# Performance work log

Hardware: AMD Instinct MI355X
Metric: run time of the kernel (lower is better)

## Reference

```python
import jax, jax.numpy as jnp
import numpy as np

B, T, D, H, C = 128, 1000, 40, 128, 8  # batch, time, input feats, hidden, classes


def _lstm_layer(x, Wih, Whh, bih, bhh):
    """Unidirectional LSTM over time. x: [B,T,Din] -> [B,T,H]. PyTorch gate order i,f,g,o."""
    Bn = x.shape[0]
    Hn = Whh.shape[1]
    b = bih + bhh
    def step(carry, xt):
        h, c = carry
        g = xt @ Wih.T + h @ Whh.T + b  # [B,4H]
        i, f, gg, o = jnp.split(g, 4, axis=-1)
        c = jax.nn.sigmoid(f) * c + jax.nn.sigmoid(i) * jnp.tanh(gg)
        h = jax.nn.sigmoid(o) * jnp.tanh(c)
        return (h, c), h
    h0 = jnp.zeros((Bn, Hn), x.dtype)
    _, hs = jax.lax.scan(step, (h0, h0), jnp.swapaxes(x, 0, 1))  # scan over time
    return jnp.swapaxes(hs, 0, 1)


def _bilstm_layer(x, pf, pb):
    fwd = _lstm_layer(x, *pf)
    bwd = jnp.flip(_lstm_layer(jnp.flip(x, 1), *pb), 1)
    return jnp.concatenate([fwd, bwd], axis=-1)  # [B,T,2H]


def setup_inputs() -> dict:
    key = jax.random.key(0)
    ks = jax.random.split(key, 16)
    s = 0.05
    def rn(k, shape):
        return jax.random.normal(k, shape, jnp.float32) * s
    inp = {"x": jax.random.normal(ks[0], (B, T, D), jnp.float32)}
    inp["ln_g"] = jnp.ones((D,), jnp.float32)
    inp["ln_b"] = jnp.zeros((D,), jnp.float32)
    dims = [D, 2 * H]  # layer-0 input feats, layer-1 input feats
    i = 1
    for l in range(2):
        for d in ("f", "b"):
            inp[f"Wih_{d}{l}"] = rn(ks[i], (4 * H, dims[l])); i += 1
            inp[f"Whh_{d}{l}"] = rn(ks[i], (4 * H, H)); i += 1
            inp[f"bih_{d}{l}"] = jnp.zeros((4 * H,), jnp.float32)
            inp[f"bhh_{d}{l}"] = jnp.zeros((4 * H,), jnp.float32)
    inp["attn_W1"] = rn(ks[i], (H, 2 * H)); i += 1
    inp["attn_b1"] = jnp.zeros((H,), jnp.float32)
    inp["attn_w2"] = rn(ks[i], (1, H)); i += 1
    inp["fc_W1"] = rn(ks[i], (H, 2 * H)); i += 1
    inp["fc_b1"] = jnp.zeros((H,), jnp.float32)
    inp["fc_W2"] = rn(ks[i], (C, H)); i += 1
    inp["fc_b2"] = jnp.zeros((C,), jnp.float32)
    return inp


def reference(x, ln_g, ln_b,
              Wih_f0, Whh_f0, bih_f0, bhh_f0, Wih_b0, Whh_b0, bih_b0, bhh_b0,
              Wih_f1, Whh_f1, bih_f1, bhh_f1, Wih_b1, Whh_b1, bih_b1, bhh_b1,
              attn_W1, attn_b1, attn_w2, fc_W1, fc_b1, fc_W2, fc_b2):
    # LayerNorm over feature dim (eps=1e-5, PyTorch default)
    mu = jnp.mean(x, axis=-1, keepdims=True)
    var = jnp.var(x, axis=-1, keepdims=True)
    xn = (x - mu) * jax.lax.rsqrt(var + 1e-5) * ln_g + ln_b
    # 2-layer bidirectional LSTM
    h = _bilstm_layer(xn, (Wih_f0, Whh_f0, bih_f0, bhh_f0), (Wih_b0, Whh_b0, bih_b0, bhh_b0))
    h = _bilstm_layer(h, (Wih_f1, Whh_f1, bih_f1, bhh_f1), (Wih_b1, Whh_b1, bih_b1, bhh_b1))
    # attention pooling: Linear-Tanh-Linear(no bias) -> softmax over time
    scores = jnp.tanh(h @ attn_W1.T + attn_b1) @ attn_w2[0]  # [B,T]
    w = jax.nn.softmax(scores, axis=1)
    ctx = jnp.einsum('bt,btd->bd', w, h)  # [B,2H]
    # MLP classifier head
    hid = jax.nn.relu(ctx @ fc_W1.T + fc_b1)
    return hid @ fc_W2.T + fc_b2  # [B,C] logits
```

## Files before the change

kernel.cpp:

```cpp
#include <hip/hip_runtime.h>

#define T_ 1000

__device__ __forceinline__ float sigf(float x) { return 1.0f / (1.0f + __expf(-x)); }
__device__ __forceinline__ float tanh_fast(float x) { return 1.0f - 2.0f / (1.0f + __expf(2.0f * x)); }
__device__ __forceinline__ float dot4(float4 a, float4 b) {
  return a.x * b.x + a.y * b.y + a.z * b.z + a.w * b.w;
}
__device__ __forceinline__ unsigned short f2bf(float f) {
  unsigned u = __float_as_uint(f);
  u = (u + 0x7fffu + ((u >> 16) & 1u)) >> 16;
  return (unsigned short)u;
}
__device__ __forceinline__ float bf2f(unsigned short h) {
  return __uint_as_float(((unsigned)h) << 16);
}
__device__ __forceinline__ float4 bf4_to_f4(ushort4 u) {
  float4 r;
  r.x = bf2f(u.x); r.y = bf2f(u.y); r.z = bf2f(u.z); r.w = bf2f(u.w);
  return r;
}

__global__ void bail_kernel(float* out, int n) {
  for (int i = threadIdx.x; i < n; i += 256) out[i] = 0.0f;
}

__global__ __launch_bounds__(512, 2) void rec0_kernel(
    const float* __restrict__ x,
    const float* __restrict__ ln_g, const float* __restrict__ ln_b,
    const float* __restrict__ Wih_f, const float* __restrict__ Whh_f,
    const float* __restrict__ bih_f, const float* __restrict__ bhh_f,
    const float* __restrict__ Wih_b, const float* __restrict__ Whh_b,
    const float* __restrict__ bih_b, const float* __restrict__ bhh_b,
    float* __restrict__ h0) {
  const int tid = threadIdx.x;
  const int j = tid & 127;
  const int p = tid >> 7;
  const int brow = blockIdx.x & 127;
  const int dir = blockIdx.x >> 7;
  const float* __restrict__ Wih = dir ? Wih_b : Wih_f;
  const float* __restrict__ Whh = dir ? Whh_b : Whh_f;
  const float* __restrict__ bih = dir ? bih_b : bih_f;
  const float* __restrict__ bhh = dir ? bhh_b : bhh_f;

  float4 wh[4][8];
  float4 wi[4][3];
#pragma unroll
  for (int g = 0; g < 4; ++g) {
    const int row = g * 128 + j;
    const float4* wr = (const float4*)(Whh + row * 128 + p * 32);
#pragma unroll
    for (int f = 0; f < 8; ++f) wh[g][f] = wr[f];
    const float* xr_ = Wih + row * 40;
#pragma unroll
    for (int f = 0; f < 3; ++f) {
      const int k0 = p * 12 + f * 4;
      float4 tv;
      tv.x = (k0 + 0 < 40) ? xr_[k0 + 0] : 0.0f;
      tv.y = (k0 + 1 < 40) ? xr_[k0 + 1] : 0.0f;
      tv.z = (k0 + 2 < 40) ? xr_[k0 + 2] : 0.0f;
      tv.w = (k0 + 3 < 40) ? xr_[k0 + 3] : 0.0f;
      wi[g][f] = tv;
    }
  }
  const float bias = bih[p * 128 + j] + bhh[p * 128 + j];
  const float b0 = (p == 0) ? bias : 0.0f;
  const float b1 = (p == 1) ? bias : 0.0f;
  const float b2 = (p == 2) ? bias : 0.0f;
  const float b3 = (p == 3) ? bias : 0.0f;

  __shared__ float4 h4[32];
  __shared__ float4 x4[12];
  __shared__ float4 part4[384];
  __shared__ float hring[8][128];

  float gj = 0.0f, bj = 0.0f;
  if (p == 1 && j < 40) { gj = ln_g[j]; bj = ln_b[j]; }

  if (tid < 32) h4[tid] = make_float4(0.f, 0.f, 0.f, 0.f);
  if (tid >= 40 && tid < 48) ((float*)x4)[tid] = 0.0f;
  __syncthreads();

  const long xbase = (long)brow * T_ * 40;
  float xr[8];
  if (p == 1 && j < 64) {
    const long tA = dir ? (T_ - 1) : 0;
    float v = (j < 40) ? x[xbase + tA * 40 + j] : 0.0f;
    float s1 = v, s2 = v * v;
#pragma unroll
    for (int m = 32; m; m >>= 1) {
      s1 += __shfl_xor(s1, m, 64);
      s2 += __shfl_xor(s2, m, 64);
    }
    const float mu = s1 * (1.0f / 40.0f);
    const float var = s2 * (1.0f / 40.0f) - mu * mu;
    const float rs = rsqrtf(var + 1e-5f);
    if (j < 40) ((float*)x4)[j] = (v - mu) * rs * gj + bj;
#pragma unroll
    for (int v8 = 0; v8 < 8; ++v8) {
      const int tr = 1 + v8;
      xr[v8] = 0.0f;
      if (j < 40 && tr < T_) {
        const long tt = dir ? (T_ - 1 - tr) : tr;
        xr[v8] = x[xbase + tt * 40 + j];
      }
    }
  }
  float c = 0.0f;
  __syncthreads();

  const long hbase = (long)brow * T_ * 256;
  for (int sb = 0; sb < 125; ++sb) {
#pragma unroll
    for (int u = 0; u < 8; ++u) {
      const int t = sb * 8 + u;
      float a0 = b0, a1 = b1, a2 = b2, a3 = b3;
#pragma unroll
      for (int f = 0; f < 3; ++f) {
        const float4 xv = x4[p * 3 + f];
        a0 += dot4(xv, wi[0][f]);
        a1 += dot4(xv, wi[1][f]);
        a2 += dot4(xv, wi[2][f]);
        a3 += dot4(xv, wi[3][f]);
      }
#pragma unroll
      for (int f = 0; f < 8; ++f) {
        const float4 hv = h4[p * 8 + f];
        a0 += dot4(hv, wh[0][f]);
        a1 += dot4(hv, wh[1][f]);
        a2 += dot4(hv, wh[2][f]);
        a3 += dot4(hv, wh[3][f]);
      }
      if (p) part4[(p - 1) * 128 + j] = make_float4(a0, a1, a2, a3);
      __syncthreads();
      if (!p) {
        const float4 q0 = part4[j], q1 = part4[128 + j], q2 = part4[256 + j];
        a0 += q0.x + q1.x + q2.x;
        a1 += q0.y + q1.y + q2.y;
        a2 += q0.z + q1.z + q2.z;
        a3 += q0.w + q1.w + q2.w;
        const float ig = sigf(a0);
        const float fg = sigf(a1);
        const float gg = tanh_fast(a2);
        const float og = sigf(a3);
        c = fg * c + ig * gg;
        const float hv = og * tanh_fast(c);
        ((float*)h4)[j] = hv;
        hring[u][j] = hv;
      } else if (p == 1 && j < 64) {
        if (t + 1 < T_) {
          float v = xr[u];
          float s1 = v, s2 = v * v;
#pragma unroll
          for (int m = 32; m; m >>= 1) {
            s1 += __shfl_xor(s1, m, 64);
            s2 += __shfl_xor(s2, m, 64);
          }
          const float mu = s1 * (1.0f / 40.0f);
          const float var = s2 * (1.0f / 40.0f) - mu * mu;
          const float rs = rsqrtf(var + 1e-5f);
          if (j < 40) ((float*)x4)[j] = (v - mu) * rs * gj + bj;
        }
      }
      __syncthreads();
      if (u == 7) {
        if (p == 3) {
#pragma unroll
          for (int v = 0; v < 8; ++v) {
            const int ts = sb * 8 + v;
            const int te = dir ? (T_ - 1 - ts) : ts;
            h0[hbase + (long)te * 256 + dir * 128 + j] = hring[v][j];
          }
        } else if (p == 1 && j < 64) {
#pragma unroll
          for (int v = 0; v < 8; ++v) {
            const int tr = sb * 8 + 9 + v;
            xr[v] = 0.0f;
            if (j < 40 && tr < T_) {
              const long tt = dir ? (T_ - 1 - tr) : tr;
              xr[v] = x[xbase + tt * 40 + j];
            }
          }
        }
      }
    }
  }
}

__global__ __launch_bounds__(512, 2) void rec1_kernel(
    const float* __restrict__ xw_f, const float* __restrict__ xw_b,
    const float* __restrict__ Whh_f, const float* __restrict__ bih_f, const float* __restrict__ bhh_f,
    const float* __restrict__ Whh_b, const float* __restrict__ bih_b, const float* __restrict__ bhh_b,
    unsigned short* __restrict__ h1b, float* __restrict__ state,
    int Tc, int t0f, int t0b, int first) {
  const int tid = threadIdx.x;
  const int j = tid & 127;
  const int p = tid >> 7;
  const int brow = blockIdx.x & 127;
  const int dir = blockIdx.x >> 7;
  const float* __restrict__ xw = dir ? xw_b : xw_f;
  const float* __restrict__ Whh = dir ? Whh_b : Whh_f;
  const float* __restrict__ bih = dir ? bih_b : bih_f;
  const float* __restrict__ bhh = dir ? bhh_b : bhh_f;
  const int t0 = dir ? t0b : t0f;

  float4 wh[4][8];
#pragma unroll
  for (int g = 0; g < 4; ++g) {
    const float4* wr = (const float4*)(Whh + (g * 128 + j) * 128 + p * 32);
#pragma unroll
    for (int f = 0; f < 8; ++f) wh[g][f] = wr[f];
  }
  const int myrow = p * 128 + j;
  const float bias = bih[myrow] + bhh[myrow];

  __shared__ float4 h4[32];
  __shared__ float4 part4[384];
  __shared__ float hring[8][128];
  float* sblk = state + (long)blockIdx.x * 256;
  float c = 0.0f;
  if (first) {
    if (tid < 32) h4[tid] = make_float4(0.f, 0.f, 0.f, 0.f);
  } else {
    if (tid < 128) ((float*)h4)[tid] = sblk[tid];
    if (!p) c = sblk[128 + j];
  }
  const long gbase = (long)brow * Tc;
  float xr[8];
#pragma unroll
  for (int v = 0; v < 8; ++v) {
    const int sn = v;
    xr[v] = 0.0f;
    if (sn < Tc) {
      const int tr = dir ? (Tc - 1 - sn) : sn;
      xr[v] = xw[(gbase + tr) * 512 + myrow];
    }
  }
  __syncthreads();

  const int nSB = (Tc + 7) / 8;
  for (int sb = 0; sb < nSB; ++sb) {
#pragma unroll
    for (int u = 0; u < 8; ++u) {
      const int s = sb * 8 + u;
      if (s >= Tc) break;
      float a0 = 0.f, a1 = 0.f, a2 = 0.f, a3 = 0.f;
#pragma unroll
      for (int f = 0; f < 8; ++f) {
        const float4 hv = h4[p * 8 + f];
        a0 += dot4(hv, wh[0][f]);
        a1 += dot4(hv, wh[1][f]);
        a2 += dot4(hv, wh[2][f]);
        a3 += dot4(hv, wh[3][f]);
      }
      const float xin = xr[u] + bias;
      if (p == 0) a0 += xin;
      else if (p == 1) a1 += xin;
      else if (p == 2) a2 += xin;
      else a3 += xin;
      if (p) part4[(p - 1) * 128 + j] = make_float4(a0, a1, a2, a3);
      __syncthreads();
      if (!p) {
        const float4 q0 = part4[j], q1 = part4[128 + j], q2 = part4[256 + j];
        a0 += q0.x + q1.x + q2.x;
        a1 += q0.y + q1.y + q2.y;
        a2 += q0.z + q1.z + q2.z;
        a3 += q0.w + q1.w + q2.w;
        const float ig = sigf(a0);
        const float fg = sigf(a1);
        const float gg = tanh_fast(a2);
        const float og = sigf(a3);
        c = fg * c + ig * gg;
        const float hv = og * tanh_fast(c);
        ((float*)h4)[j] = hv;
        hring[u][j] = hv;
      }
      __syncthreads();
      if (u == 7 || s + 1 == Tc) {
        if (p == 3) {
#pragma unroll
          for (int v = 0; v < 8; ++v) {
            const int s2 = sb * 8 + v;
            if (s2 <= s) {
              const int tt = dir ? (Tc - 1 - s2) : s2;
              h1b[((long)brow * T_ + (t0 + tt)) * 256 + dir * 128 + j] = f2bf(hring[v][j]);
            }
          }
        }
#pragma unroll
        for (int v = 0; v < 8; ++v) {
          const int sn = s + 1 + v;
          xr[v] = 0.0f;
          if (sn < Tc) {
            const int tr = dir ? (Tc - 1 - sn) : sn;
            xr[v] = xw[(gbase + tr) * 512 + myrow];
          }
        }
      }
    }
  }
  if (tid < 128) sblk[tid] = ((float*)h4)[tid];
  if (!p) sblk[128 + j] = c;
}

__global__ __launch_bounds__(256, 2) void gemm_xw1(
    const float* __restrict__ h0,
    const float* __restrict__ Wf, const float* __restrict__ Wb,
    float* __restrict__ xwf, float* __restrict__ xwb,
    int Tc, int t0f, int t0b) {
  __shared__ float As[64 * 36];
  __shared__ float Bs[128 * 36];
  __shared__ int rowbase[64];
  const int tid = threadIdx.x;
  const int tx = tid & 15, ty = tid >> 4;
  const int r0 = blockIdx.x * 64;
  const int jt = blockIdx.y;
  const int dir = jt >> 2;
  const int nh = jt & 3;
  const float* __restrict__ W = dir ? Wb : Wf;
  float* __restrict__ out = dir ? xwb : xwf;
  const int jbase = nh * 128;
  const int t0 = dir ? t0b : t0f;

  if (tid < 64) {
    const int r = r0 + tid;
    const int br = r / Tc;
    rowbase[tid] = br * T_ + t0 + (r - br * Tc);
  }

  float4* As4 = (float4*)As;
  float4* Bs4 = (float4*)Bs;
  float acc[4][8] = {};
#pragma unroll 1
  for (int kk = 0; kk < 8; ++kk) {
    __syncthreads();
#pragma unroll
    for (int i = 0; i < 2; ++i) {
      const int q = tid + i * 256;
      const int row = q >> 3, k4 = q & 7;
      As4[row * 9 + k4] = *(const float4*)&h0[(long)rowbase[row] * 256 + kk * 32 + k4 * 4];
    }
#pragma unroll
    for (int i = 0; i < 4; ++i) {
      const int q = tid + i * 256;
      const int row = q >> 3, k4 = q & 7;
      Bs4[row * 9 + k4] = *(const float4*)&W[(long)(jbase + row) * 256 + kk * 32 + k4 * 4];
    }
    __syncthreads();
#pragma unroll 1
    for (int k4 = 0; k4 < 8; ++k4) {
      float4 av[4];
#pragma unroll
      for (int r = 0; r < 4; ++r) av[r] = As4[(ty * 4 + r) * 9 + k4];
#pragma unroll
      for (int c2 = 0; c2 < 8; ++c2) {
        const float4 bv = Bs4[(tx + 16 * c2) * 9 + k4];
#pragma unroll
        for (int r = 0; r < 4; ++r) acc[r][c2] += dot4(av[r], bv);
      }
    }
  }
#pragma unroll
  for (int r = 0; r < 4; ++r) {
    const long ob = (long)(r0 + ty * 4 + r) * 512 + jbase + tx;
#pragma unroll
    for (int c2 = 0; c2 < 8; ++c2) out[ob + c2 * 16] = acc[r][c2];
  }
}

__global__ __launch_bounds__(256, 2) void score_kernel(
    const unsigned short* __restrict__ h1b, const float* __restrict__ W1,
    const float* __restrict__ b1, const float* __restrict__ w2,
    float* __restrict__ scores) {
  __shared__ float As[64 * 36];
  __shared__ float Bs[128 * 36];
  const int tid = threadIdx.x;
  const int tx = tid & 15, ty = tid >> 4;
  const long r0 = (long)blockIdx.x * 64;

  float4* As4 = (float4*)As;
  float4* Bs4 = (float4*)Bs;
  float acc[4][8] = {};
#pragma unroll 1
  for (int kk = 0; kk < 8; ++kk) {
    __syncthreads();
#pragma unroll
    for (int i = 0; i < 2; ++i) {
      const int q = tid + i * 256;
      const int row = q >> 3, k4 = q & 7;
      const ushort4 uv = *(const ushort4*)&h1b[(r0 + row) * 256 + kk * 32 + k4 * 4];
      As4[row * 9 + k4] = bf4_to_f4(uv);
    }
#pragma unroll
    for (int i = 0; i < 4; ++i) {
      const int q = tid + i * 256;
      const int row = q >> 3, k4 = q & 7;
      Bs4[row * 9 + k4] = *(const float4*)&W1[(long)row * 256 + kk * 32 + k4 * 4];
    }
    __syncthreads();
#pragma unroll 1
    for (int k4 = 0; k4 < 8; ++k4) {
      float4 av[4];
#pragma unroll
      for (int r = 0; r < 4; ++r) av[r] = As4[(ty * 4 + r) * 9 + k4];
#pragma unroll
      for (int c2 = 0; c2 < 8; ++c2) {
        const float4 bv = Bs4[(tx + 16 * c2) * 9 + k4];
#pragma unroll
        for (int r = 0; r < 4; ++r) acc[r][c2] += dot4(av[r], bv);
      }
    }
  }
#pragma unroll
  for (int r = 0; r < 4; ++r) {
    float s = 0.0f;
#pragma unroll
    for (int c2 = 0; c2 < 8; ++c2) {
      const int col = tx + 16 * c2;
      s += tanh_fast(acc[r][c2] + b1[col]) * w2[col];
    }
#pragma unroll
    for (int m = 1; m < 16; m <<= 1) s += __shfl_xor(s, m, 16);
    if (tx == 0) scores[r0 + ty * 4 + r] = s;
  }
}

__global__ __launch_bounds__(256, 2) void head_kernel(
    const float* __restrict__ scores, const unsigned short* __restrict__ h1b,
    const float* __restrict__ fW1, const float* __restrict__ fb1,
    const float* __restrict__ fW2, const float* __restrict__ fb2,
    float* __restrict__ outp) {
  const int b = blockIdx.x, tid = threadIdx.x;
  __shared__ float wls[1000];
  __shared__ float red[8];
  __shared__ __align__(16) float ctx[256];
  __shared__ __align__(16) float hid[128];

  float sv[4];
  float mx = -1e30f;
#pragma unroll
  for (int i = 0; i < 4; ++i) {
    const int t = tid + i * 256;
    sv[i] = (t < 1000) ? scores[b * 1000 + t] : -1e30f;
    mx = fmaxf(mx, sv[i]);
  }
  for (int m = 32; m; m >>= 1) mx = fmaxf(mx, __shfl_xor(mx, m, 64));
  if ((tid & 63) == 0) red[tid >> 6] = mx;
  __syncthreads();
  mx = fmaxf(fmaxf(red[0], red[1]), fmaxf(red[2], red[3]));
  float se = 0.0f;
#pragma unroll
  for (int i = 0; i < 4; ++i) {
    const int t = tid + i * 256;
    if (t < 1000) {
      const float e = __expf(sv[i] - mx);
      wls[t] = e;
      se += e;
    }
  }
  for (int m = 32; m; m >>= 1) se += __shfl_xor(se, m, 64);
  if ((tid & 63) == 0) red[4 + (tid >> 6)] = se;
  __syncthreads();
  const float rinv = 1.0f / (red[4] + red[5] + red[6] + red[7]);

  float a = 0.0f;
  const unsigned short* hb = h1b + (long)b * T_ * 256 + tid;
  for (int t = 0; t < T_; ++t) a = fmaf(wls[t], bf2f(hb[t * 256]), a);
  ctx[tid] = a * rinv;
  __syncthreads();
  if (tid < 128) {
    float s = fb1[tid];
    const float4* wr = (const float4*)&fW1[tid * 256];
    const float4* cc = (const float4*)ctx;
#pragma unroll
    for (int f = 0; f < 64; ++f) s += dot4(wr[f], cc[f]);
    hid[tid] = fmaxf(s, 0.0f);
  }
  __syncthreads();
  if (tid < 8) {
    float s = fb2[tid];
    const float4* wr = (const float4*)&fW2[tid * 128];
    const float4* hh = (const float4*)hid;
#pragma unroll
    for (int f = 0; f < 32; ++f) s += dot4(wr[f], hh[f]);
    outp[b * 8 + tid] = s;
  }
}

extern "C" void kernel_launch(void* const* d_in, const int* in_sizes, int n_in,
                              void* d_out, int out_size, void* d_ws, size_t ws_size,
                              hipStream_t stream) {
  (void)in_sizes; (void)n_in; (void)out_size;
  const float* x       = (const float*)d_in[0];
  const float* ln_g    = (const float*)d_in[1];
  const float* ln_b    = (const float*)d_in[2];
  const float* Wih_f0  = (const float*)d_in[3];
  const float* Whh_f0  = (const float*)d_in[4];
  const float* bih_f0  = (const float*)d_in[5];
  const float* bhh_f0  = (const float*)d_in[6];
  const float* Wih_b0  = (const float*)d_in[7];
  const float* Whh_b0  = (const float*)d_in[8];
  const float* bih_b0  = (const float*)d_in[9];
  const float* bhh_b0  = (const float*)d_in[10];
  const float* Wih_f1  = (const float*)d_in[11];
  const float* Whh_f1  = (const float*)d_in[12];
  const float* bih_f1  = (const float*)d_in[13];
  const float* bhh_f1  = (const float*)d_in[14];
  const float* Wih_b1  = (const float*)d_in[15];
  const float* Whh_b1  = (const float*)d_in[16];
  const float* bih_b1  = (const float*)d_in[17];
  const float* bhh_b1  = (const float*)d_in[18];
  const float* attn_W1 = (const float*)d_in[19];
  const float* attn_b1 = (const float*)d_in[20];
  const float* attn_w2 = (const float*)d_in[21];
  const float* fc_W1   = (const float*)d_in[22];
  const float* fc_b1   = (const float*)d_in[23];
  const float* fc_W2   = (const float*)d_in[24];
  const float* fc_b2   = (const float*)d_in[25];

  char* base = (char*)d_ws;
  size_t off = 0;
  auto alloc = [&](size_t bytes) {
    char* ptr = base + off;
    off += (bytes + 255) & ~(size_t)255;
    return ptr;
  };
  float*          h0    = (float*)alloc(32768000ull * 4);
  unsigned short* h1b   = (unsigned short*)alloc(32768000ull * 2);
  float*          state = (float*)alloc(65536ull * 4);
  float*          scor  = (float*)alloc(128000ull * 4);

  const size_t rem = (ws_size > off) ? (ws_size - off) : 0;
  static const int cands[16] = {1000, 500, 250, 200, 125, 100, 50, 40, 25, 20, 10, 8, 5, 4, 2, 1};
  int Tc = 0;
  for (int ci = 0; ci < 16; ++ci) {
    if (524288ull * (size_t)cands[ci] <= rem) { Tc = cands[ci]; break; }
  }
  if (Tc == 0) {
    bail_kernel<<<dim3(1), dim3(256), 0, stream>>>((float*)d_out, 1024);
    return;
  }
  float* xwf = (float*)(base + off);
  float* xwb = xwf + 65536L * Tc;

  rec0_kernel<<<dim3(256), dim3(512), 0, stream>>>(x, ln_g, ln_b,
                                                   Wih_f0, Whh_f0, bih_f0, bhh_f0,
                                                   Wih_b0, Whh_b0, bih_b0, bhh_b0, h0);
  const int nch = T_ / Tc;
  for (int ch = 0; ch < nch; ++ch) {
    const int t0f = ch * Tc;
    const int t0b = T_ - (ch + 1) * Tc;
    gemm_xw1<<<dim3(2 * Tc, 8), dim3(256), 0, stream>>>(h0, Wih_f1, Wih_b1, xwf, xwb, Tc, t0f, t0b);
    rec1_kernel<<<dim3(256), dim3(512), 0, stream>>>(xwf, xwb, Whh_f1, bih_f1, bhh_f1,
                                                     Whh_b1, bih_b1, bhh_b1, h1b, state,
                                                     Tc, t0f, t0b, (ch == 0) ? 1 : 0);
  }
  score_kernel<<<dim3(2000), dim3(256), 0, stream>>>(h1b, attn_W1, attn_b1, attn_w2, scor);
  head_kernel<<<dim3(128), dim3(256), 0, stream>>>(scor, h1b, fc_W1, fc_b1, fc_W2, fc_b2,
                                                   (float*)d_out);
}
```

Measured before the change: 3.589 ms.

## Reduce LSTM gate partials with wave shuffles, precompute LayerNorm stats, packed FMA

The recurrent kernels now give each hidden unit to four adjacent lanes that split the K dimension. Their partial gate sums are combined with shuffle-xor instead of a shared-memory partial buffer and an extra barrier, which leaves one __syncthreads per timestep instead of two. LayerNorm mean and rstd are computed up front by a new kernel, and the gamma/beta terms are folded into the input weights and bias. x is prefetched through double-buffered shared rings, and h write-back is spread over all threads. Dot products use packed v2f FMAs in the recurrent and GEMM kernels, and the launch bounds drop to 1 block per SM, which may reduce occupancy.

```diff
diff --git a/kernel.cpp b/kernel.cpp
--- a/kernel.cpp
+++ b/kernel.cpp
@@ -1,12 +1,22 @@
 #include <hip/hip_runtime.h>
 
 #define T_ 1000
+
+typedef float v2f __attribute__((ext_vector_type(2)));
 
 __device__ __forceinline__ float sigf(float x) { return 1.0f / (1.0f + __expf(-x)); }
 __device__ __forceinline__ float tanh_fast(float x) { return 1.0f - 2.0f / (1.0f + __expf(2.0f * x)); }
 __device__ __forceinline__ float dot4(float4 a, float4 b) {
   return a.x * b.x + a.y * b.y + a.z * b.z + a.w * b.w;
 }
+__device__ __forceinline__ void pkfma(v2f& acc, float4 w, float4 v) {
+  v2f wl; wl[0] = w.x; wl[1] = w.y;
+  v2f wh; wh[0] = w.z; wh[1] = w.w;
+  v2f vl; vl[0] = v.x; vl[1] = v.y;
+  v2f vh; vh[0] = v.z; vh[1] = v.w;
+  acc += wl * vl;
+  acc += wh * vh;
+}
 __device__ __forceinline__ unsigned short f2bf(float f) {
   unsigned u = __float_as_uint(f);
   u = (u + 0x7fffu + ((u >> 16) & 1u)) >> 16;
@@ -25,8 +35,29 @@
   for (int i = threadIdx.x; i < n; i += 256) out[i] = 0.0f;
 }
 
-__global__ __launch_bounds__(512, 2) void rec0_kernel(
+__global__ __launch_bounds__(256) void ln_stats_kernel(const float* __restrict__ x,
+                                                       float* __restrict__ mu_arr,
+                                                       float* __restrict__ rs_arr) {
+  const int lane = threadIdx.x & 63;
+  const int w = threadIdx.x >> 6;
+  const long row = (long)blockIdx.x * 4 + w;
+  float v = (lane < 40) ? x[row * 40 + lane] : 0.0f;
+  float s1 = v, s2 = v * v;
+  for (int m = 32; m; m >>= 1) {
+    s1 += __shfl_xor(s1, m, 64);
+    s2 += __shfl_xor(s2, m, 64);
+  }
+  if (lane == 0) {
+    const float mu = s1 * (1.0f / 40.0f);
+    const float var = s2 * (1.0f / 40.0f) - mu * mu;
+    mu_arr[row] = mu;
+    rs_arr[row] = rsqrtf(var + 1e-5f);
+  }
+}
+
+__global__ __launch_bounds__(512, 1) void rec0_kernel(
     const float* __restrict__ x,
+    const float* __restrict__ mu_arr, const float* __restrict__ rs_arr,
     const float* __restrict__ ln_g, const float* __restrict__ ln_b,
     const float* __restrict__ Wih_f, const float* __restrict__ Whh_f,
     const float* __restrict__ bih_f, const float* __restrict__ bhh_f,
@@ -34,8 +65,8 @@
     const float* __restrict__ bih_b, const float* __restrict__ bhh_b,
     float* __restrict__ h0) {
   const int tid = threadIdx.x;
-  const int j = tid & 127;
-  const int p = tid >> 7;
+  const int u = (tid >> 6) * 16 + ((tid & 63) >> 2);
+  const int p = tid & 3;
   const int brow = blockIdx.x & 127;
   const int dir = blockIdx.x >> 7;
   const float* __restrict__ Wih = dir ? Wih_b : Wih_f;
@@ -45,157 +76,165 @@
 
   float4 wh[4][8];
   float4 wi[4][3];
+  float S1[4], bias[4];
 #pragma unroll
   for (int g = 0; g < 4; ++g) {
-    const int row = g * 128 + j;
+    const int row = g * 128 + u;
     const float4* wr = (const float4*)(Whh + row * 128 + p * 32);
 #pragma unroll
-    for (int f = 0; f < 8; ++f) wh[g][f] = wr[f];
-    const float* xr_ = Wih + row * 40;
+    for (int ff = 0; ff < 8; ++ff) wh[g][ff] = wr[(ff + 2 * p) & 7];
+    float s1p = 0.0f, s2p = 0.0f;
 #pragma unroll
     for (int f = 0; f < 3; ++f) {
-      const int k0 = p * 12 + f * 4;
-      float4 tv;
-      tv.x = (k0 + 0 < 40) ? xr_[k0 + 0] : 0.0f;
-      tv.y = (k0 + 1 < 40) ? xr_[k0 + 1] : 0.0f;
-      tv.z = (k0 + 2 < 40) ? xr_[k0 + 2] : 0.0f;
-      tv.w = (k0 + 3 < 40) ? xr_[k0 + 3] : 0.0f;
-      wi[g][f] = tv;
-    }
-  }
-  const float bias = bih[p * 128 + j] + bhh[p * 128 + j];
-  const float b0 = (p == 0) ? bias : 0.0f;
-  const float b1 = (p == 1) ? bias : 0.0f;
-  const float b2 = (p == 2) ? bias : 0.0f;
-  const float b3 = (p == 3) ? bias : 0.0f;
-
-  __shared__ float4 h4[32];
-  __shared__ float4 x4[12];
-  __shared__ float4 part4[384];
-  __shared__ float hring[8][128];
-
-  float gj = 0.0f, bj = 0.0f;
-  if (p == 1 && j < 40) { gj = ln_g[j]; bj = ln_b[j]; }
-
-  if (tid < 32) h4[tid] = make_float4(0.f, 0.f, 0.f, 0.f);
-  if (tid >= 40 && tid < 48) ((float*)x4)[tid] = 0.0f;
+      float tmp[4];
+#pragma unroll
+      for (int e = 0; e < 4; ++e) {
+        const int k = p * 12 + f * 4 + e;
+        const float wv = (k < 40) ? Wih[row * 40 + k] : 0.0f;
+        const float gk = (k < 40) ? ln_g[k] : 0.0f;
+        const float bk = (k < 40) ? ln_b[k] : 0.0f;
+        const float wf = wv * gk;
+        tmp[e] = wf;
+        s1p += wf;
+        s2p += wv * bk;
+      }
+      wi[g][f] = make_float4(tmp[0], tmp[1], tmp[2], tmp[3]);
+    }
+    s1p += __shfl_xor(s1p, 1, 64); s1p += __shfl_xor(s1p, 2, 64);
+    s2p += __shfl_xor(s2p, 1, 64); s2p += __shfl_xor(s2p, 2, 64);
+    S1[g] = s1p;
+    bias[g] = bih[g * 128 + u] + bhh[g * 128 + u] + s2p;
+  }
+
+  __shared__ float h4f[128];
+  __shared__ __align__(16) float x_ring[2][8][48];
+  __shared__ float mu_ring[2][8], rs_ring[2][8];
+  __shared__ float hring[2][8][128];
+
+  const int lr8 = tid / 40;
+  const int lcol = tid - lr8 * 40;
+  const long xbase = (long)brow * T_ * 40;
+  const long mbase = (long)brow * T_;
+  const long hbase = (long)brow * T_ * 256;
+
+  if (tid < 128) h4f[tid] = 0.0f;
+  if (tid < 128) {
+    const int b = tid >> 6, r = (tid >> 3) & 7, cc = 40 + (tid & 7);
+    x_ring[b][r][cc] = 0.0f;
+  }
+  if (tid < 320) {
+    const int t = lr8;
+    const int tt = dir ? (T_ - 1 - t) : t;
+    x_ring[0][lr8][lcol] = x[xbase + (long)tt * 40 + lcol];
+  } else if (tid < 328) {
+    const int t = tid - 320;
+    const int tt = dir ? (T_ - 1 - t) : t;
+    mu_ring[0][t] = mu_arr[mbase + tt];
+  } else if (tid < 336) {
+    const int t = tid - 328;
+    const int tt = dir ? (T_ - 1 - t) : t;
+    rs_ring[0][t] = rs_arr[mbase + tt];
+  }
+  float c = 0.0f;
+  float xpf = 0.0f, mupf = 0.0f, rspf = 0.0f;
   __syncthreads();
 
-  const long xbase = (long)brow * T_ * 40;
-  float xr[8];
-  if (p == 1 && j < 64) {
-    const long tA = dir ? (T_ - 1) : 0;
-    float v = (j < 40) ? x[xbase + tA * 40 + j] : 0.0f;
-    float s1 = v, s2 = v * v;
-#pragma unroll
-    for (int m = 32; m; m >>= 1) {
-      s1 += __shfl_xor(s1, m, 64);
-      s2 += __shfl_xor(s2, m, 64);
-    }
-    const float mu = s1 * (1.0f / 40.0f);
-    const float var = s2 * (1.0f / 40.0f) - mu * mu;
-    const float rs = rsqrtf(var + 1e-5f);
-    if (j < 40) ((float*)x4)[j] = (v - mu) * rs * gj + bj;
-#pragma unroll
-    for (int v8 = 0; v8 < 8; ++v8) {
-      const int tr = 1 + v8;
-      xr[v8] = 0.0f;
-      if (j < 40 && tr < T_) {
-        const long tt = dir ? (T_ - 1 - tr) : tr;
-        xr[v8] = x[xbase + tt * 40 + j];
-      }
-    }
-  }
-  float c = 0.0f;
-  __syncthreads();
-
-  const long hbase = (long)brow * T_ * 256;
   for (int sb = 0; sb < 125; ++sb) {
-#pragma unroll
-    for (int u = 0; u < 8; ++u) {
-      const int t = sb * 8 + u;
-      float a0 = b0, a1 = b1, a2 = b2, a3 = b3;
-#pragma unroll
-      for (int f = 0; f < 3; ++f) {
-        const float4 xv = x4[p * 3 + f];
-        a0 += dot4(xv, wi[0][f]);
-        a1 += dot4(xv, wi[1][f]);
-        a2 += dot4(xv, wi[2][f]);
-        a3 += dot4(xv, wi[3][f]);
-      }
-#pragma unroll
-      for (int f = 0; f < 8; ++f) {
-        const float4 hv = h4[p * 8 + f];
-        a0 += dot4(hv, wh[0][f]);
-        a1 += dot4(hv, wh[1][f]);
-        a2 += dot4(hv, wh[2][f]);
-        a3 += dot4(hv, wh[3][f]);
-      }
-      if (p) part4[(p - 1) * 128 + j] = make_float4(a0, a1, a2, a3);
-      __syncthreads();
-      if (!p) {
-        const float4 q0 = part4[j], q1 = part4[128 + j], q2 = part4[256 + j];
-        a0 += q0.x + q1.x + q2.x;
-        a1 += q0.y + q1.y + q2.y;
-        a2 += q0.z + q1.z + q2.z;
-        a3 += q0.w + q1.w + q2.w;
-        const float ig = sigf(a0);
-        const float fg = sigf(a1);
-        const float gg = tanh_fast(a2);
-        const float og = sigf(a3);
-        c = fg * c + ig * gg;
-        const float hv = og * tanh_fast(c);
-        ((float*)h4)[j] = hv;
-        hring[u][j] = hv;
-      } else if (p == 1 && j < 64) {
-        if (t + 1 < T_) {
-          float v = xr[u];
-          float s1 = v, s2 = v * v;
-#pragma unroll
-          for (int m = 32; m; m >>= 1) {
-            s1 += __shfl_xor(s1, m, 64);
-            s2 += __shfl_xor(s2, m, 64);
-          }
-          const float mu = s1 * (1.0f / 40.0f);
-          const float var = s2 * (1.0f / 40.0f) - mu * mu;
-          const float rs = rsqrtf(var + 1e-5f);
-          if (j < 40) ((float*)x4)[j] = (v - mu) * rs * gj + bj;
-        }
-      }
-      __syncthreads();
-      if (u == 7) {
-        if (p == 3) {
-#pragma unroll
-          for (int v = 0; v < 8; ++v) {
-            const int ts = sb * 8 + v;
-            const int te = dir ? (T_ - 1 - ts) : ts;
-            h0[hbase + (long)te * 256 + dir * 128 + j] = hring[v][j];
-          }
-        } else if (p == 1 && j < 64) {
-#pragma unroll
-          for (int v = 0; v < 8; ++v) {
-            const int tr = sb * 8 + 9 + v;
-            xr[v] = 0.0f;
-            if (j < 40 && tr < T_) {
-              const long tt = dir ? (T_ - 1 - tr) : tr;
-              xr[v] = x[xbase + tt * 40 + j];
-            }
+    const int rb = sb & 1;
+#pragma unroll
+    for (int su = 0; su < 8; ++su) {
+      if (su == 0) {
+        if (sb + 1 < 125) {
+          if (tid < 320) {
+            const int t = (sb + 1) * 8 + lr8;
+            const int tt = dir ? (T_ - 1 - t) : t;
+            xpf = x[xbase + (long)tt * 40 + lcol];
+          } else if (tid < 328) {
+            const int t = (sb + 1) * 8 + (tid - 320);
+            const int tt = dir ? (T_ - 1 - t) : t;
+            mupf = mu_arr[mbase + tt];
+          } else if (tid < 336) {
+            const int t = (sb + 1) * 8 + (tid - 328);
+            const int tt = dir ? (T_ - 1 - t) : t;
+            rspf = rs_arr[mbase + tt];
           }
         }
-      }
-    }
-  }
-}
-
-__global__ __launch_bounds__(512, 2) void rec1_kernel(
+        if (sb > 0) {
+#pragma unroll
+          for (int e = 0; e < 2; ++e) {
+            const int idx = tid + e * 512;
+            const int v = idx >> 7, j = idx & 127;
+            const int ts = (sb - 1) * 8 + v;
+            const int te = dir ? (T_ - 1 - ts) : ts;
+            h0[hbase + (long)te * 256 + dir * 128 + j] = hring[rb ^ 1][v][j];
+          }
+        }
+      }
+      v2f hacc[4], xacc[4];
+#pragma unroll
+      for (int g = 0; g < 4; ++g) { hacc[g] = 0.0f; xacc[g] = 0.0f; }
+      const float4* h4v = (const float4*)h4f;
+#pragma unroll
+      for (int ff = 0; ff < 8; ++ff) {
+        const float4 hv = h4v[p * 8 + ((ff + 2 * p) & 7)];
+        pkfma(hacc[0], wh[0][ff], hv);
+        pkfma(hacc[1], wh[1][ff], hv);
+        pkfma(hacc[2], wh[2][ff], hv);
+        pkfma(hacc[3], wh[3][ff], hv);
+      }
+      const float4* xr4 = (const float4*)x_ring[rb][su];
+#pragma unroll
+      for (int f = 0; f < 3; ++f) {
+        const float4 xv = xr4[p * 3 + f];
+        pkfma(xacc[0], wi[0][f], xv);
+        pkfma(xacc[1], wi[1][f], xv);
+        pkfma(xacc[2], wi[2][f], xv);
+        pkfma(xacc[3], wi[3][f], xv);
+      }
+      const float rs = rs_ring[rb][su];
+      const float mu = mu_ring[rb][su];
+      float pg[4];
+#pragma unroll
+      for (int g = 0; g < 4; ++g) {
+        pg[g] = (hacc[g][0] + hacc[g][1]) + rs * (xacc[g][0] + xacc[g][1]);
+        pg[g] += __shfl_xor(pg[g], 1, 64);
+        pg[g] += __shfl_xor(pg[g], 2, 64);
+        pg[g] += bias[g] - rs * mu * S1[g];
+      }
+      const float ig = sigf(pg[0]);
+      const float fg = sigf(pg[1]);
+      const float gg = tanh_fast(pg[2]);
+      const float og = sigf(pg[3]);
+      c = fg * c + ig * gg;
+      const float hv = og * tanh_fast(c);
+      if (p == 0) { h4f[u] = hv; hring[rb][su][u] = hv; }
+      if (su == 7 && sb + 1 < 125) {
+        if (tid < 320) x_ring[rb ^ 1][lr8][lcol] = xpf;
+        else if (tid < 328) mu_ring[rb ^ 1][tid - 320] = mupf;
+        else if (tid < 336) rs_ring[rb ^ 1][tid - 328] = rspf;
+      }
+      __syncthreads();
+    }
+  }
+#pragma unroll
+  for (int e = 0; e < 2; ++e) {
+    const int idx = tid + e * 512;
+    const int v = idx >> 7, j = idx & 127;
+    const int ts = 124 * 8 + v;
+    const int te = dir ? (T_ - 1 - ts) : ts;
+    h0[hbase + (long)te * 256 + dir * 128 + j] = hring[0][v][j];
+  }
+}
+
+__global__ __launch_bounds__(512, 1) void rec1_kernel(
     const float* __restrict__ xw_f, const float* __restrict__ xw_b,
     const float* __restrict__ Whh_f, const float* __restrict__ bih_f, const float* __restrict__ bhh_f,
     const float* __restrict__ Whh_b, const float* __restrict__ bih_b, const float* __restrict__ bhh_b,
     unsigned short* __restrict__ h1b, float* __restrict__ state,
     int Tc, int t0f, int t0b, int first) {
   const int tid = threadIdx.x;
-  const int j = tid & 127;
-  const int p = tid >> 7;
+  const int u = (tid >> 6) * 16 + ((tid & 63) >> 2);
+  const int p = tid & 3;
   const int brow = blockIdx.x & 127;
   const int dir = blockIdx.x >> 7;
   const float* __restrict__ xw = dir ? xw_b : xw_f;
@@ -207,32 +246,30 @@
   float4 wh[4][8];
 #pragma unroll
   for (int g = 0; g < 4; ++g) {
-    const float4* wr = (const float4*)(Whh + (g * 128 + j) * 128 + p * 32);
-#pragma unroll
-    for (int f = 0; f < 8; ++f) wh[g][f] = wr[f];
-  }
-  const int myrow = p * 128 + j;
-  const float bias = bih[myrow] + bhh[myrow];
-
-  __shared__ float4 h4[32];
-  __shared__ float4 part4[384];
-  __shared__ float hring[8][128];
+    const float4* wr = (const float4*)(Whh + (g * 128 + u) * 128 + p * 32);
+#pragma unroll
+    for (int ff = 0; ff < 8; ++ff) wh[g][ff] = wr[(ff + 2 * p) & 7];
+  }
+  const int myrow = p * 128 + u;
+  const float bias_p = bih[myrow] + bhh[myrow];
+
+  __shared__ float h4f[128];
+  __shared__ float hring[2][8][128];
   float* sblk = state + (long)blockIdx.x * 256;
   float c = 0.0f;
   if (first) {
-    if (tid < 32) h4[tid] = make_float4(0.f, 0.f, 0.f, 0.f);
+    if (tid < 128) h4f[tid] = 0.0f;
   } else {
-    if (tid < 128) ((float*)h4)[tid] = sblk[tid];
-    if (!p) c = sblk[128 + j];
+    if (tid < 128) h4f[tid] = sblk[tid];
+    c = sblk[128 + u];
   }
   const long gbase = (long)brow * Tc;
   float xr[8];
 #pragma unroll
   for (int v = 0; v < 8; ++v) {
-    const int sn = v;
     xr[v] = 0.0f;
-    if (sn < Tc) {
-      const int tr = dir ? (Tc - 1 - sn) : sn;
+    if (v < Tc) {
+      const int tr = dir ? (Tc - 1 - v) : v;
       xr[v] = xw[(gbase + tr) * 512 + myrow];
     }
   }
@@ -240,53 +277,49 @@
 
   const int nSB = (Tc + 7) / 8;
   for (int sb = 0; sb < nSB; ++sb) {
-#pragma unroll
-    for (int u = 0; u < 8; ++u) {
-      const int s = sb * 8 + u;
+    const int rb = sb & 1;
+#pragma unroll
+    for (int su = 0; su < 8; ++su) {
+      const int s = sb * 8 + su;
       if (s >= Tc) break;
-      float a0 = 0.f, a1 = 0.f, a2 = 0.f, a3 = 0.f;
-#pragma unroll
-      for (int f = 0; f < 8; ++f) {
-        const float4 hv = h4[p * 8 + f];
-        a0 += dot4(hv, wh[0][f]);
-        a1 += dot4(hv, wh[1][f]);
-        a2 += dot4(hv, wh[2][f]);
-        a3 += dot4(hv, wh[3][f]);
-      }
-      const float xin = xr[u] + bias;
-      if (p == 0) a0 += xin;
-      else if (p == 1) a1 += xin;
-      else if (p == 2) a2 += xin;
-      else a3 += xin;
-      if (p) part4[(p - 1) * 128 + j] = make_float4(a0, a1, a2, a3);
-      __syncthreads();
-      if (!p) {
-        const float4 q0 = part4[j], q1 = part4[128 + j], q2 = part4[256 + j];
-        a0 += q0.x + q1.x + q2.x;
-        a1 += q0.y + q1.y + q2.y;
-        a2 += q0.z + q1.z + q2.z;
-        a3 += q0.w + q1.w + q2.w;
-        const float ig = sigf(a0);
-        const float fg = sigf(a1);
-        const float gg = tanh_fast(a2);
-        const float og = sigf(a3);
-        c = fg * c + ig * gg;
-        const float hv = og * tanh_fast(c);
-        ((float*)h4)[j] = hv;
-        hring[u][j] = hv;
-      }
-      __syncthreads();
-      if (u == 7 || s + 1 == Tc) {
-        if (p == 3) {
-#pragma unroll
-          for (int v = 0; v < 8; ++v) {
-            const int s2 = sb * 8 + v;
-            if (s2 <= s) {
-              const int tt = dir ? (Tc - 1 - s2) : s2;
-              h1b[((long)brow * T_ + (t0 + tt)) * 256 + dir * 128 + j] = f2bf(hring[v][j]);
-            }
-          }
+      if (su == 0 && sb > 0) {
+#pragma unroll
+        for (int e = 0; e < 2; ++e) {
+          const int idx = tid + e * 512;
+          const int v = idx >> 7, j = idx & 127;
+          const int s2 = (sb - 1) * 8 + v;
+          const int tt = dir ? (Tc - 1 - s2) : s2;
+          h1b[((long)brow * T_ + (t0 + tt)) * 256 + dir * 128 + j] = f2bf(hring[rb ^ 1][v][j]);
         }
+      }
+      v2f hacc[4];
+#pragma unroll
+      for (int g = 0; g < 4; ++g) hacc[g] = 0.0f;
+      const float4* h4v = (const float4*)h4f;
+#pragma unroll
+      for (int ff = 0; ff < 8; ++ff) {
+        const float4 hv = h4v[p * 8 + ((ff + 2 * p) & 7)];
+        pkfma(hacc[0], wh[0][ff], hv);
+        pkfma(hacc[1], wh[1][ff], hv);
+        pkfma(hacc[2], wh[2][ff], hv);
+        pkfma(hacc[3], wh[3][ff], hv);
+      }
+      const float xin = xr[su] + bias_p;
+      float pg[4];
+#pragma unroll
+      for (int g = 0; g < 4; ++g) {
+        pg[g] = hacc[g][0] + hacc[g][1] + ((p == g) ? xin : 0.0f);
+        pg[g] += __shfl_xor(pg[g], 1, 64);
+        pg[g] += __shfl_xor(pg[g], 2, 64);
+      }
+      const float ig = sigf(pg[0]);
+      const float fg = sigf(pg[1]);
+      const float gg = tanh_fast(pg[2]);
+      const float og = sigf(pg[3]);
+      c = fg * c + ig * gg;
+      const float hv = og * tanh_fast(c);
+      if (p == 0) { h4f[u] = hv; hring[rb][su][u] = hv; }
+      if (su == 7) {
 #pragma unroll
         for (int v = 0; v < 8; ++v) {
           const int sn = s + 1 + v;
@@ -297,10 +330,26 @@
           }
         }
       }
-    }
-  }
-  if (tid < 128) sblk[tid] = ((float*)h4)[tid];
-  if (!p) sblk[128 + j] = c;
+      __syncthreads();
+    }
+  }
+  {
+    const int sbL = (Tc - 1) >> 3;
+    const int cnt = Tc - sbL * 8;
+    const int rbL = sbL & 1;
+#pragma unroll
+    for (int e = 0; e < 2; ++e) {
+      const int idx = tid + e * 512;
+      const int v = idx >> 7, j = idx & 127;
+      if (v < cnt) {
+        const int s2 = sbL * 8 + v;
+        const int tt = dir ? (Tc - 1 - s2) : s2;
+        h1b[((long)brow * T_ + (t0 + tt)) * 256 + dir * 128 + j] = f2bf(hring[rbL][v][j]);
+      }
+    }
+  }
+  if (tid < 128) sblk[tid] = h4f[tid];
+  if (p == 0) sblk[128 + u] = c;
 }
 
 __global__ __launch_bounds__(256, 2) void gemm_xw1(
@@ -330,7 +379,11 @@
 
   float4* As4 = (float4*)As;
   float4* Bs4 = (float4*)Bs;
-  float acc[4][8] = {};
+  v2f acc2[4][8];
+#pragma unroll
+  for (int r = 0; r < 4; ++r)
+#pragma unroll
+    for (int c2 = 0; c2 < 8; ++c2) acc2[r][c2] = 0.0f;
 #pragma unroll 1
   for (int kk = 0; kk < 8; ++kk) {
     __syncthreads();
@@ -356,7 +409,7 @@
       for (int c2 = 0; c2 < 8; ++c2) {
         const float4 bv = Bs4[(tx + 16 * c2) * 9 + k4];
 #pragma unroll
-        for (int r = 0; r < 4; ++r) acc[r][c2] += dot4(av[r], bv);
+        for (int r = 0; r < 4; ++r) pkfma(acc2[r][c2], av[r], bv);
       }
     }
   }
@@ -364,7 +417,7 @@
   for (int r = 0; r < 4; ++r) {
     const long ob = (long)(r0 + ty * 4 + r) * 512 + jbase + tx;
 #pragma unroll
-    for (int c2 = 0; c2 < 8; ++c2) out[ob + c2 * 16] = acc[r][c2];
+    for (int c2 = 0; c2 < 8; ++c2) out[ob + c2 * 16] = acc2[r][c2][0] + acc2[r][c2][1];
   }
 }
 
@@ -380,7 +433,11 @@
 
   float4* As4 = (float4*)As;
   float4* Bs4 = (float4*)Bs;
-  float acc[4][8] = {};
+  v2f acc2[4][8];
+#pragma unroll
+  for (int r = 0; r < 4; ++r)
+#pragma unroll
+    for (int c2 = 0; c2 < 8; ++c2) acc2[r][c2] = 0.0f;
 #pragma unroll 1
   for (int kk = 0; kk < 8; ++kk) {
     __syncthreads();
@@ -407,7 +464,7 @@
       for (int c2 = 0; c2 < 8; ++c2) {
         const float4 bv = Bs4[(tx + 16 * c2) * 9 + k4];
 #pragma unroll
-        for (int r = 0; r < 4; ++r) acc[r][c2] += dot4(av[r], bv);
+        for (int r = 0; r < 4; ++r) pkfma(acc2[r][c2], av[r], bv);
       }
     }
   }
@@ -417,7 +474,7 @@
 #pragma unroll
     for (int c2 = 0; c2 < 8; ++c2) {
       const int col = tx + 16 * c2;
-      s += tanh_fast(acc[r][c2] + b1[col]) * w2[col];
+      s += tanh_fast(acc2[r][c2][0] + acc2[r][c2][1] + b1[col]) * w2[col];
     }
 #pragma unroll
     for (int m = 1; m < 16; m <<= 1) s += __shfl_xor(s, m, 16);
@@ -529,6 +586,8 @@
   unsigned short* h1b   = (unsigned short*)alloc(32768000ull * 2);
   float*          state = (float*)alloc(65536ull * 4);
   float*          scor  = (float*)alloc(128000ull * 4);
+  float*          mu_a  = (float*)alloc(128000ull * 4);
+  float*          rs_a  = (float*)alloc(128000ull * 4);
 
   const size_t rem = (ws_size > off) ? (ws_size - off) : 0;
   static const int cands[16] = {1000, 500, 250, 200, 125, 100, 50, 40, 25, 20, 10, 8, 5, 4, 2, 1};
@@ -543,7 +602,8 @@
   float* xwf = (float*)(base + off);
   float* xwb = xwf + 65536L * Tc;
 
-  rec0_kernel<<<dim3(256), dim3(512), 0, stream>>>(x, ln_g, ln_b,
+  ln_stats_kernel<<<dim3(32000), dim3(256), 0, stream>>>(x, mu_a, rs_a);
+  rec0_kernel<<<dim3(256), dim3(512), 0, stream>>>(x, mu_a, rs_a, ln_g, ln_b,
                                                    Wih_f0, Whh_f0, bih_f0, bhh_f0,
                                                    Wih_b0, Whh_b0, bih_b0, bhh_b0, h0);
   const int nch = T_ / Tc;
```

New measurement: 2.887 ms. 19.5% less time.
